# Kernel tuning notes

Hardware: AMD Instinct MI355X
Metric: run time of the kernel (lower is better)

Reference implementation:

```python
import jax, jax.numpy as jnp
import numpy as np

B, S, D = 4, 4096, 256


def setup_inputs() -> dict:
    key = jax.random.key(0)
    ks = jax.random.split(key, 7)
    s = 1.0 / np.sqrt(D)
    return {
        "x": jax.random.normal(ks[0], (B, S, D), dtype=jnp.float32),
        "Wq": jax.random.normal(ks[1], (D, D), dtype=jnp.float32) * s,
        "bq": jax.random.normal(ks[2], (D,), dtype=jnp.float32) * s,
        "Wk": jax.random.normal(ks[3], (D, D), dtype=jnp.float32) * s,
        "bk": jax.random.normal(ks[4], (D,), dtype=jnp.float32) * s,
        "Wv": jax.random.normal(ks[5], (D, D), dtype=jnp.float32) * s,
        "bv": jax.random.normal(ks[6], (D,), dtype=jnp.float32) * s,
    }


def reference(x, Wq, bq, Wk, bk, Wv, bv):
    # QKV projections (torch Linear: y = x @ W^T + b; here W stored as [in, out])
    Q = jax.nn.relu(jnp.einsum("bsd,df->bsf", x, Wq) + bq)  # [B,S,D]
    K = jax.nn.relu(jnp.einsum("bsd,df->bsf", x, Wk) + bk)  # [B,S,D]
    V = jnp.einsum("bsd,df->bsf", x, Wv) + bv               # [B,S,D]
    scores = jnp.einsum("bqd,bkd->bqk", Q, K)               # [B,S,S], no 1/sqrt(d) scaling (as in source)
    attn = jax.nn.softmax(scores, axis=-1)
    return jnp.einsum("bqk,bkd->bqd", attn, V)              # [B,S,D]
```

## Files before the change

kernel.cpp:

```cpp
#include <hip/hip_runtime.h>
#include <stdint.h>

typedef __bf16 bf16;
typedef bf16 bf16x8 __attribute__((ext_vector_type(8)));
typedef _Float16 f16;
typedef f16 f16x8 __attribute__((ext_vector_type(8)));
typedef f16 f16x4 __attribute__((ext_vector_type(4)));
typedef float f32x4 __attribute__((ext_vector_type(4)));
typedef float f32x16 __attribute__((ext_vector_type(16)));
typedef unsigned short u16;
typedef unsigned int u32;
typedef u32 u32x2 __attribute__((ext_vector_type(2)));
typedef u16 u16x8v __attribute__((ext_vector_type(8)));

#define LOG2E 1.44269504088896340736f

__device__ __forceinline__ u16 f2bf(float f) {
  u32 u = __float_as_uint(f);
  u32 r = u + 0x7fffu + ((u >> 16) & 1u);
  return (u16)(r >> 16);
}
__device__ __forceinline__ float bf2f(u16 h) { return __uint_as_float(((u32)h) << 16); }

__device__ __forceinline__ u32 pkrtz(float a, float b) {
  auto r = __builtin_amdgcn_cvt_pkrtz(a, b);
  u32 u; __builtin_memcpy(&u, &r, 4);
  return u;
}
__device__ __forceinline__ float xmax32(float v) {
  u32x2 r = __builtin_amdgcn_permlane32_swap(__float_as_uint(v), __float_as_uint(v), false, false);
  return fmaxf(__uint_as_float(r[0]), __uint_as_float(r[1]));
}
__device__ __forceinline__ float xsum32(float v) {
  u32x2 r = __builtin_amdgcn_permlane32_swap(__float_as_uint(v), __float_as_uint(v), false, false);
  return __uint_as_float(r[0]) + __uint_as_float(r[1]);
}

union ABu { u16x8v u; bf16x8 b; };
union PAu { u32 w[4]; f16x8 v; };

__global__ void wt_kernel(const float* __restrict__ Wq, const float* __restrict__ Wk,
                          const float* __restrict__ Wv, u16* __restrict__ Wh,
                          u16* __restrict__ Wl) {
  int w = blockIdx.x >> 4;
  int chunk = blockIdx.x & 15;
  const float* W = (w == 0) ? Wq : (w == 1) ? Wk : Wv;
  int t = threadIdx.x;
  int o = chunk * 16 + (t & 15);
  int i0 = (t >> 4) * 16;
  u16x8v h0, h1, l0, l1;
  #pragma unroll
  for (int ii = 0; ii < 8; ++ii) {
    float v0 = W[(size_t)(i0 + ii) * 256 + o];
    u16 h = f2bf(v0); h0[ii] = h; l0[ii] = f2bf(v0 - bf2f(h));
    float v1 = W[(size_t)(i0 + 8 + ii) * 256 + o];
    h = f2bf(v1); h1[ii] = h; l1[ii] = f2bf(v1 - bf2f(h));
  }
  size_t base = (size_t)w * 65536 + (size_t)o * 256 + i0;
  *(u16x8v*)(Wh + base) = h0; *(u16x8v*)(Wh + base + 8) = h1;
  *(u16x8v*)(Wl + base) = l0; *(u16x8v*)(Wl + base + 8) = l1;
}

__global__ __launch_bounds__(256, 2) void proj_kernel(
    const float* __restrict__ x, const float* __restrict__ bq,
    const float* __restrict__ bk, const float* __restrict__ bv,
    const u16* __restrict__ Wh, const u16* __restrict__ Wl,
    f16* __restrict__ Qf, f16* __restrict__ Kf, f16* __restrict__ Vt) {
  __shared__ __align__(16) char Whs[16384];
  __shared__ __align__(16) char Wls[16384];

  int m = blockIdx.x, w = blockIdx.y;
  int tid = threadIdx.x, lane = tid & 63, wv = tid >> 6;
  int r = lane & 15, c = lane >> 4;
  int row0 = m * 128 + wv * 32;
  const char* Whw = (const char*)(Wh + (size_t)w * 65536);
  const char* Wlw = (const char*)(Wl + (size_t)w * 65536);
  const float* bias = (w == 0) ? bq : (w == 1) ? bk : bv;

  f32x4 acc[2][16];
  #pragma unroll
  for (int g = 0; g < 2; ++g)
    #pragma unroll
    for (int n = 0; n < 16; ++n) acc[g][n] = (f32x4)0.0f;

  for (int ks = 0; ks < 8; ++ks) {
    if (ks) __syncthreads();
    #pragma unroll
    for (int ss = 0; ss < 4; ++ss) {
      int slot = ss * 256 + tid;
      int row = slot >> 2, c4 = slot & 3;
      int dby = (c4 << 4) ^ (((row >> 1) & 3) << 4);
      const char* gh = Whw + (size_t)row * 512 + ks * 64 + dby;
      const char* gl = Wlw + (size_t)row * 512 + ks * 64 + dby;
      __builtin_amdgcn_global_load_lds(
          (const __attribute__((address_space(1))) void*)gh,
          (__attribute__((address_space(3))) void*)(Whs + slot * 16), 16, 0, 0);
      __builtin_amdgcn_global_load_lds(
          (const __attribute__((address_space(1))) void*)gl,
          (__attribute__((address_space(3))) void*)(Wls + slot * 16), 16, 0, 0);
    }
    __syncthreads();

    ABu ah[2], al[2];
    #pragma unroll
    for (int g = 0; g < 2; ++g) {
      const float* xrow = x + (size_t)(row0 + g * 16 + r) * 256 + ks * 32 + c * 8;
      float4 a0 = *(const float4*)(xrow);
      float4 a1 = *(const float4*)(xrow + 4);
      float xv[8] = {a0.x, a0.y, a0.z, a0.w, a1.x, a1.y, a1.z, a1.w};
      #pragma unroll
      for (int j = 0; j < 8; ++j) {
        u16 h = f2bf(xv[j]);
        ah[g].u[j] = h;
        al[g].u[j] = f2bf(xv[j] - bf2f(h));
      }
    }
    #pragma unroll
    for (int n = 0; n < 16; ++n) {
      int wrow = n * 16 + r;
      int wof = (c * 16) ^ (((wrow >> 1) & 3) << 4);
      bf16x8 whf = *(const bf16x8*)(Whs + wrow * 64 + wof);
      bf16x8 wlf = *(const bf16x8*)(Wls + wrow * 64 + wof);
      #pragma unroll
      for (int g = 0; g < 2; ++g) {
        acc[g][n] = __builtin_amdgcn_mfma_f32_16x16x32_bf16(ah[g].b, whf, acc[g][n], 0, 0, 0);
        acc[g][n] = __builtin_amdgcn_mfma_f32_16x16x32_bf16(al[g].b, whf, acc[g][n], 0, 0, 0);
        acc[g][n] = __builtin_amdgcn_mfma_f32_16x16x32_bf16(ah[g].b, wlf, acc[g][n], 0, 0, 0);
      }
    }
  }

  if (w < 2) {
    f16* outp = (w == 0) ? Qf : Kf;
    float osc = (w == 0) ? LOG2E : 1.0f;
    #pragma unroll
    for (int g = 0; g < 2; ++g)
      #pragma unroll
      for (int n = 0; n < 16; ++n) {
        int col = n * 16 + r;
        float bb = bias[col];
        #pragma unroll
        for (int i = 0; i < 4; ++i) {
          float v = fmaxf(acc[g][n][i] + bb, 0.0f) * osc;
          outp[(size_t)(row0 + g * 16 + c * 4 + i) * 256 + col] = (f16)v;
        }
      }
  } else {
    #pragma unroll
    for (int g = 0; g < 2; ++g) {
      int grow = row0 + g * 16 + c * 4;
      int b = grow >> 12, s0 = grow & 4095;
      #pragma unroll
      for (int n = 0; n < 16; ++n) {
        int d = n * 16 + r;
        float bb = bias[d];
        f16x4 pk;
        #pragma unroll
        for (int i = 0; i < 4; ++i) pk[i] = (f16)(acc[g][n][i] + bb);
        *(f16x4*)(Vt + (size_t)(b * 256 + d) * 4096 + s0) = pk;
      }
    }
  }
}

__global__ __launch_bounds__(256, 2) void attn_kernel(
    const f16* __restrict__ Qf, const f16* __restrict__ Kf,
    const f16* __restrict__ Vt, f16* __restrict__ Opart, float* __restrict__ Ml) {
  __shared__ __align__(16) char Ksm[2][16384];
  __shared__ __align__(16) char Vsm[2][16384];

  int bid = blockIdx.x;
  int xcd = bid & 7;
  int batch = xcd >> 1;
  int kq = ((xcd & 1) << 1) | ((bid >> 3) & 1);
  int qtl = bid >> 4;
  int tid = threadIdx.x, lane = tid & 63, wv = tid >> 6;
  int ln = lane & 31, hi = lane >> 5;
  int q0 = qtl * 128 + wv * 32;
  int kv0 = kq * 1024;

  f16x8 qf[16];
  {
    const f16* qp = Qf + ((size_t)(batch * 4096 + q0 + ln)) * 256 + hi * 8;
    #pragma unroll
    for (int ks = 0; ks < 16; ++ks) qf[ks] = *(const f16x8*)(qp + ks * 16);
  }

  f32x16 O[8];
  #pragma unroll
  for (int dt = 0; dt < 8; ++dt) O[dt] = (f32x16)0.0f;
  float m_ = -1.0e30f, l_ = 0.0f;

  const char* Kbase = (const char*)(Kf + ((size_t)(batch * 4096 + kv0)) * 256);
  const char* Vbase = (const char*)(Vt + (size_t)batch * 1048576 + kv0);

#define STAGE(T, BF)                                                           \
  {                                                                            \
    _Pragma("unroll")                                                          \
    for (int rr = 0; rr < 4; ++rr) {                                           \
      int slot = rr * 256 + tid;                                               \
      int krow = slot >> 5;                                                    \
      int dby = ((slot & 31) << 4) ^ ((krow & 7) << 4);                        \
      const char* g = Kbase + (size_t)((T) * 32 + krow) * 512 + dby;           \
      __builtin_amdgcn_global_load_lds(                                        \
          (const __attribute__((address_space(1))) void*)g,                    \
          (__attribute__((address_space(3))) void*)(Ksm[BF] + slot * 16), 16, 0, 0); \
    }                                                                          \
    _Pragma("unroll")                                                          \
    for (int rr = 0; rr < 4; ++rr) {                                           \
      int slot = rr * 256 + tid;                                               \
      int vrow = slot >> 2;                                                    \
      int dby = ((slot & 3) << 4) ^ (((vrow >> 1) & 3) << 4);                  \
      const char* g = Vbase + (size_t)vrow * 8192 + (T) * 64 + dby;            \
      __builtin_amdgcn_global_load_lds(                                        \
          (const __attribute__((address_space(1))) void*)g,                    \
          (__attribute__((address_space(3))) void*)(Vsm[BF] + slot * 16), 16, 0, 0); \
    }                                                                          \
  }

  int kswz = (ln & 7) << 4;
  int vswz = ((ln >> 1) & 3) << 4;
  int hi16 = hi * 16;

  STAGE(0, 0);

  for (int t = 0; t < 32; ++t) {
    __builtin_amdgcn_s_barrier();
    if (t < 31) {
      STAGE(t + 1, (t + 1) & 1);
      asm volatile("s_waitcnt vmcnt(8)" ::: "memory");
    } else {
      asm volatile("s_waitcnt vmcnt(0)" ::: "memory");
    }
    __builtin_amdgcn_sched_barrier(0);
    __builtin_amdgcn_s_barrier();

    const char* Kc = Ksm[t & 1];
    const char* Vc = Vsm[t & 1];

    f32x16 sA = (f32x16)0.0f;
    __builtin_amdgcn_s_setprio(1);
    #pragma unroll
    for (int ks = 0; ks < 16; ++ks) {
      f16x8 kf = *(const f16x8*)(Kc + ln * 512 + ((ks * 32 + hi16) ^ kswz));
      sA = __builtin_amdgcn_mfma_f32_32x32x16_f16(kf, qf[ks], sA, 0, 0, 0);
    }
    __builtin_amdgcn_s_setprio(0);

    float pm = fmaxf(
        fmaxf(fmaxf(fmaxf(sA[0], sA[1]), fmaxf(sA[2], sA[3])),
              fmaxf(fmaxf(sA[4], sA[5]), fmaxf(sA[6], sA[7]))),
        fmaxf(fmaxf(fmaxf(sA[8], sA[9]), fmaxf(sA[10], sA[11])),
              fmaxf(fmaxf(sA[12], sA[13]), fmaxf(sA[14], sA[15]))));
    pm = xmax32(pm);
    if (!__all(pm <= m_ + 11.5416f)) {
      float mn = fmaxf(m_, pm);
      float sc = exp2f(m_ - mn);
      m_ = mn; l_ *= sc;
      #pragma unroll
      for (int rg = 0; rg < 16; ++rg) {
        float srg = __shfl(sc, (rg & 3) + 8 * (rg >> 2) + 4 * hi);
        #pragma unroll
        for (int dt = 0; dt < 8; ++dt) O[dt][rg] *= srg;
      }
    }
    float p_[16];
    #pragma unroll
    for (int j = 0; j < 16; ++j) p_[j] = exp2f(sA[j] - m_);
    float ps = (((p_[0] + p_[1]) + (p_[2] + p_[3])) +
                ((p_[4] + p_[5]) + (p_[6] + p_[7]))) +
               (((p_[8] + p_[9]) + (p_[10] + p_[11])) +
                ((p_[12] + p_[13]) + (p_[14] + p_[15])));
    l_ += xsum32(ps);

    PAu pa0, pa1;
    {
      u32x2 r1 = __builtin_amdgcn_permlane32_swap(pkrtz(p_[0], p_[1]), pkrtz(p_[4], p_[5]), false, false);
      u32x2 r2 = __builtin_amdgcn_permlane32_swap(pkrtz(p_[2], p_[3]), pkrtz(p_[6], p_[7]), false, false);
      pa0.w[0] = r1[0]; pa0.w[1] = r2[0]; pa0.w[2] = r1[1]; pa0.w[3] = r2[1];
      u32x2 r3 = __builtin_amdgcn_permlane32_swap(pkrtz(p_[8], p_[9]), pkrtz(p_[12], p_[13]), false, false);
      u32x2 r4 = __builtin_amdgcn_permlane32_swap(pkrtz(p_[10], p_[11]), pkrtz(p_[14], p_[15]), false, false);
      pa1.w[0] = r3[0]; pa1.w[1] = r4[0]; pa1.w[2] = r3[1]; pa1.w[3] = r4[1];
    }

    __builtin_amdgcn_s_setprio(1);
    #pragma unroll
    for (int ks = 0; ks < 16; ++ks) {
      int dt = ks >> 1, k2 = ks & 1;
      f16x8 vf = *(const f16x8*)(Vc + (dt * 32 + ln) * 64 + ((k2 * 32 + hi16) ^ vswz));
      O[dt] = __builtin_amdgcn_mfma_f32_32x32x16_f16(k2 ? pa1.v : pa0.v, vf, O[dt], 0, 0, 0);
    }
    __builtin_amdgcn_s_setprio(0);
  }

  float invl = 1.0f / l_;
  #pragma unroll
  for (int rg = 0; rg < 16; ++rg) {
    int qr = (rg & 3) + 8 * (rg >> 2) + 4 * hi;
    float iv = __shfl(invl, qr);
    size_t row = (size_t)kq * 16384 + batch * 4096 + q0 + qr;
    #pragma unroll
    for (int dt = 0; dt < 8; ++dt)
      Opart[row * 256 + dt * 32 + ln] = (f16)(O[dt][rg] * iv);
  }
  if (hi == 0) {
    size_t grow = (size_t)kq * 16384 + batch * 4096 + q0 + ln;
    Ml[grow * 2] = m_;
    Ml[grow * 2 + 1] = l_;
  }
#undef STAGE
}

__global__ __launch_bounds__(256) void merge_kernel(
    const f16* __restrict__ Opart, const float* __restrict__ Ml,
    float* __restrict__ out) {
  int gid = blockIdx.x * 256 + threadIdx.x;
  int row = gid >> 5, d0 = (gid & 31) * 8;
  float m[4], l[4];
  #pragma unroll
  for (int p = 0; p < 4; ++p) {
    m[p] = Ml[((size_t)p * 16384 + row) * 2];
    l[p] = Ml[((size_t)p * 16384 + row) * 2 + 1];
  }
  float M = fmaxf(fmaxf(m[0], m[1]), fmaxf(m[2], m[3]));
  float wl[4], L = 0.f;
  #pragma unroll
  for (int p = 0; p < 4; ++p) { wl[p] = exp2f(m[p] - M) * l[p]; L += wl[p]; }
  float o[8] = {0.f, 0.f, 0.f, 0.f, 0.f, 0.f, 0.f, 0.f};
  #pragma unroll
  for (int p = 0; p < 4; ++p) {
    f16x8 v = *(const f16x8*)(Opart + ((size_t)p * 16384 + row) * 256 + d0);
    #pragma unroll
    for (int j = 0; j < 8; ++j) o[j] += wl[p] * (float)v[j];
  }
  float invL = 1.0f / L;
  float4 o0 = {o[0] * invL, o[1] * invL, o[2] * invL, o[3] * invL};
  float4 o1 = {o[4] * invL, o[5] * invL, o[6] * invL, o[7] * invL};
  *(float4*)(out + (size_t)row * 256 + d0) = o0;
  *(float4*)(out + (size_t)row * 256 + d0 + 4) = o1;
}

extern "C" void kernel_launch(void* const* d_in, const int* in_sizes, int n_in,
                              void* d_out, int out_size, void* d_ws, size_t ws_size,
                              hipStream_t stream) {
  const float* x  = (const float*)d_in[0];
  const float* Wq = (const float*)d_in[1];
  const float* bq = (const float*)d_in[2];
  const float* Wk = (const float*)d_in[3];
  const float* bk = (const float*)d_in[4];
  const float* Wv = (const float*)d_in[5];
  const float* bv = (const float*)d_in[6];
  float* out = (float*)d_out;

  u16* Wh = (u16*)d_ws;
  u16* Wl = Wh + 3 * 65536;
  f16* Qf = (f16*)(Wl + 3 * 65536);
  f16* Kf = Qf + (size_t)16384 * 256;
  f16* Vt = Kf + (size_t)16384 * 256;
  f16* Opart = Vt + (size_t)4 * 256 * 4096;
  float* Ml = (float*)(Opart + (size_t)4 * 16384 * 256);

  wt_kernel<<<48, 256, 0, stream>>>(Wq, Wk, Wv, Wh, Wl);
  proj_kernel<<<dim3(128, 3), 256, 0, stream>>>(x, bq, bk, bv, Wh, Wl, Qf, Kf, Vt);
  attn_kernel<<<512, 256, 0, stream>>>(Qf, Kf, Vt, Opart, Ml);
  merge_kernel<<<2048, 256, 0, stream>>>(Opart, Ml, out);
}
```

Before: 167.2 us.

## Load V fragments straight from global in a fragment-major layout, drop V LDS staging

The projection kernel now writes V in a fragment-major layout, blocked by 16 keys and then by feature column. This lets each attention wave read its MFMA B-operand fragments directly from global memory into registers, so the V shared-memory buffers and their async copies are removed and only K stays double-buffered in LDS. The attention block also grows to 8 waves covering 256 queries, which halves the block count so each staged K tile is shared by more waves. In exchange, every wave re-reads the same V tile through the caches. Register pressure also rises sharply, since 16 V fragment vectors are now live alongside the Q fragments and O accumulators under a 512-thread launch bound, so spills or lower occupancy are possible.

Result: slower. 198.7 us (+18.9%).

```diff
diff --git a/kernel.cpp b/kernel.cpp
--- a/kernel.cpp
+++ b/kernel.cpp
@@ -65,7 +65,7 @@
     const float* __restrict__ x, const float* __restrict__ bq,
     const float* __restrict__ bk, const float* __restrict__ bv,
     const u16* __restrict__ Wh, const u16* __restrict__ Wl,
-    f16* __restrict__ Qf, f16* __restrict__ Kf, f16* __restrict__ Vt) {
+    f16* __restrict__ Qf, f16* __restrict__ Kf, f16* __restrict__ Vw) {
   __shared__ __align__(16) char Whs[16384];
   __shared__ __align__(16) char Wls[16384];
 
@@ -150,6 +150,7 @@
     for (int g = 0; g < 2; ++g) {
       int grow = row0 + g * 16 + c * 4;
       int b = grow >> 12, s0 = grow & 4095;
+      int kb = s0 >> 4, k16 = s0 & 15;
       #pragma unroll
       for (int n = 0; n < 16; ++n) {
         int d = n * 16 + r;
@@ -157,17 +158,16 @@
         f16x4 pk;
         #pragma unroll
         for (int i = 0; i < 4; ++i) pk[i] = (f16)(acc[g][n][i] + bb);
-        *(f16x4*)(Vt + (size_t)(b * 256 + d) * 4096 + s0) = pk;
-      }
-    }
-  }
-}
-
-__global__ __launch_bounds__(256, 2) void attn_kernel(
+        *(f16x4*)(Vw + (((size_t)b * 256 + kb) * 256 + d) * 16 + k16) = pk;
+      }
+    }
+  }
+}
+
+__global__ __launch_bounds__(512, 2) void attn_kernel(
     const f16* __restrict__ Qf, const f16* __restrict__ Kf,
-    const f16* __restrict__ Vt, f16* __restrict__ Opart, float* __restrict__ Ml) {
+    const f16* __restrict__ Vw, f16* __restrict__ Opart, float* __restrict__ Ml) {
   __shared__ __align__(16) char Ksm[2][16384];
-  __shared__ __align__(16) char Vsm[2][16384];
 
   int bid = blockIdx.x;
   int xcd = bid & 7;
@@ -176,7 +176,7 @@
   int qtl = bid >> 4;
   int tid = threadIdx.x, lane = tid & 63, wv = tid >> 6;
   int ln = lane & 31, hi = lane >> 5;
-  int q0 = qtl * 128 + wv * 32;
+  int q0 = qtl * 256 + wv * 32;
   int kv0 = kq * 1024;
 
   f16x8 qf[16];
@@ -192,13 +192,13 @@
   float m_ = -1.0e30f, l_ = 0.0f;
 
   const char* Kbase = (const char*)(Kf + ((size_t)(batch * 4096 + kv0)) * 256);
-  const char* Vbase = (const char*)(Vt + (size_t)batch * 1048576 + kv0);
+  const f16* Vlane = Vw + ((size_t)batch * 256 * 256) * 16 + (size_t)ln * 16 + hi * 8;
 
 #define STAGE(T, BF)                                                           \
   {                                                                            \
     _Pragma("unroll")                                                          \
-    for (int rr = 0; rr < 4; ++rr) {                                           \
-      int slot = rr * 256 + tid;                                               \
+    for (int rr = 0; rr < 2; ++rr) {                                           \
+      int slot = rr * 512 + tid;                                               \
       int krow = slot >> 5;                                                    \
       int dby = ((slot & 31) << 4) ^ ((krow & 7) << 4);                        \
       const char* g = Kbase + (size_t)((T) * 32 + krow) * 512 + dby;           \
@@ -206,20 +206,9 @@
           (const __attribute__((address_space(1))) void*)g,                    \
           (__attribute__((address_space(3))) void*)(Ksm[BF] + slot * 16), 16, 0, 0); \
     }                                                                          \
-    _Pragma("unroll")                                                          \
-    for (int rr = 0; rr < 4; ++rr) {                                           \
-      int slot = rr * 256 + tid;                                               \
-      int vrow = slot >> 2;                                                    \
-      int dby = ((slot & 3) << 4) ^ (((vrow >> 1) & 3) << 4);                  \
-      const char* g = Vbase + (size_t)vrow * 8192 + (T) * 64 + dby;            \
-      __builtin_amdgcn_global_load_lds(                                        \
-          (const __attribute__((address_space(1))) void*)g,                    \
-          (__attribute__((address_space(3))) void*)(Vsm[BF] + slot * 16), 16, 0, 0); \
-    }                                                                          \
   }
 
   int kswz = (ln & 7) << 4;
-  int vswz = ((ln >> 1) & 3) << 4;
   int hi16 = hi * 16;
 
   STAGE(0, 0);
@@ -228,7 +217,7 @@
     __builtin_amdgcn_s_barrier();
     if (t < 31) {
       STAGE(t + 1, (t + 1) & 1);
-      asm volatile("s_waitcnt vmcnt(8)" ::: "memory");
+      asm volatile("s_waitcnt vmcnt(2)" ::: "memory");
     } else {
       asm volatile("s_waitcnt vmcnt(0)" ::: "memory");
     }
@@ -236,7 +225,11 @@
     __builtin_amdgcn_s_barrier();
 
     const char* Kc = Ksm[t & 1];
-    const char* Vc = Vsm[t & 1];
+    size_t vrow0 = ((size_t)(kq * 64 + t * 2) * 256) * 16;
+    f16x8 vA[8];
+    #pragma unroll
+    for (int dt = 0; dt < 8; ++dt)
+      vA[dt] = *(const f16x8*)(Vlane + vrow0 + (size_t)dt * 512);
 
     f32x16 sA = (f32x16)0.0f;
     __builtin_amdgcn_s_setprio(1);
@@ -285,11 +278,20 @@
 
     __builtin_amdgcn_s_setprio(1);
     #pragma unroll
-    for (int ks = 0; ks < 16; ++ks) {
-      int dt = ks >> 1, k2 = ks & 1;
-      f16x8 vf = *(const f16x8*)(Vc + (dt * 32 + ln) * 64 + ((k2 * 32 + hi16) ^ vswz));
-      O[dt] = __builtin_amdgcn_mfma_f32_32x32x16_f16(k2 ? pa1.v : pa0.v, vf, O[dt], 0, 0, 0);
-    }
+    for (int dt = 0; dt < 4; ++dt)
+      O[dt] = __builtin_amdgcn_mfma_f32_32x32x16_f16(pa0.v, vA[dt], O[dt], 0, 0, 0);
+    __builtin_amdgcn_s_setprio(0);
+    f16x8 vB[8];
+    #pragma unroll
+    for (int dt = 0; dt < 8; ++dt)
+      vB[dt] = *(const f16x8*)(Vlane + vrow0 + 4096 + (size_t)dt * 512);
+    __builtin_amdgcn_s_setprio(1);
+    #pragma unroll
+    for (int dt = 4; dt < 8; ++dt)
+      O[dt] = __builtin_amdgcn_mfma_f32_32x32x16_f16(pa0.v, vA[dt], O[dt], 0, 0, 0);
+    #pragma unroll
+    for (int dt = 0; dt < 8; ++dt)
+      O[dt] = __builtin_amdgcn_mfma_f32_32x32x16_f16(pa1.v, vB[dt], O[dt], 0, 0, 0);
     __builtin_amdgcn_s_setprio(0);
   }
 
@@ -356,12 +358,12 @@
   u16* Wl = Wh + 3 * 65536;
   f16* Qf = (f16*)(Wl + 3 * 65536);
   f16* Kf = Qf + (size_t)16384 * 256;
-  f16* Vt = Kf + (size_t)16384 * 256;
-  f16* Opart = Vt + (size_t)4 * 256 * 4096;
+  f16* Vw = Kf + (size_t)16384 * 256;
+  f16* Opart = Vw + (size_t)4 * 256 * 4096;
   float* Ml = (float*)(Opart + (size_t)4 * 16384 * 256);
 
   wt_kernel<<<48, 256, 0, stream>>>(Wq, Wk, Wv, Wh, Wl);
-  proj_kernel<<<dim3(128, 3), 256, 0, stream>>>(x, bq, bk, bv, Wh, Wl, Qf, Kf, Vt);
-  attn_kernel<<<512, 256, 0, stream>>>(Qf, Kf, Vt, Opart, Ml);
+  proj_kernel<<<dim3(128, 3), 256, 0, stream>>>(x, bq, bk, bv, Wh, Wl, Qf, Kf, Vw);
+  attn_kernel<<<256, 512, 0, stream>>>(Qf, Kf, Vw, Opart, Ml);
   merge_kernel<<<2048, 256, 0, stream>>>(Opart, Ml, out);
 }
```
